# Kernel optimization log

Hardware: AMD Instinct MI355X
Metric: run time of the kernel (lower is better)

## Reference

```python
import jax, jax.numpy as jnp
import numpy as np

N = 8192        # num_drugs
D_EMB = 256     # args.gcn_hidden3 (global encoder input)
D_FEAT = 256    # args.hidden_size (local encoder input)
H1 = H2 = H3 = 256  # args.ff_hidden1/2/3
LOG2 = float(np.log(2.0))
ADJ_DENSITY = 0.01


def _ff(x, w1, b1, w2, b2, w3, b3, ws, bs):
    # FF block: 3-layer ReLU MLP + linear shortcut (FF_local / FF_global)
    h = jax.nn.relu(x @ w1 + b1)
    h = jax.nn.relu(h @ w2 + b2)
    h = jax.nn.relu(h @ w3 + b3)
    return h + x @ ws + bs


def _lin_init(k, fan_in, fan_out):
    s = 1.0 / np.sqrt(fan_in)
    kw, kb = jax.random.split(k)
    w = jax.random.uniform(kw, (fan_in, fan_out), minval=-s, maxval=s, dtype=jnp.float32)
    b = jax.random.uniform(kb, (fan_out,), minval=-s, maxval=s, dtype=jnp.float32)
    return w, b


def setup_inputs() -> dict:
    key = jax.random.key(0)
    ks = jax.random.split(key, 11)
    g_w1, g_b1 = _lin_init(ks[0], D_EMB, H1)
    g_w2, g_b2 = _lin_init(ks[1], H1, H2)
    g_w3, g_b3 = _lin_init(ks[2], H2, H3)
    g_ws, g_bs = _lin_init(ks[3], D_EMB, H3)
    l_w1, l_b1 = _lin_init(ks[4], D_FEAT, H1)
    l_w2, l_b2 = _lin_init(ks[5], H1, H2)
    l_w3, l_b3 = _lin_init(ks[6], H2, H3)
    l_ws, l_bs = _lin_init(ks[7], D_FEAT, H3)
    embeddings = jax.random.normal(ks[8], (N, D_EMB), dtype=jnp.float32)
    features = jax.random.normal(ks[9], (N, D_FEAT), dtype=jnp.float32)
    adj_tensor = (jax.random.uniform(ks[10], (N, N)) < ADJ_DENSITY).astype(jnp.float32)
    return dict(embeddings=embeddings, features=features, adj_tensor=adj_tensor,
                num_drugs=N,
                g_w1=g_w1, g_b1=g_b1, g_w2=g_w2, g_b2=g_b2, g_w3=g_w3, g_b3=g_b3,
                g_ws=g_ws, g_bs=g_bs,
                l_w1=l_w1, l_b1=l_b1, l_w2=l_w2, l_b2=l_b2, l_w3=l_w3, l_b3=l_b3,
                l_ws=l_ws, l_bs=l_bs)


def reference(embeddings, features, adj_tensor,
              g_w1, g_b1, g_w2, g_b2, g_w3, g_b3, g_ws, g_bs,
              l_w1, l_b1, l_w2, l_b2, l_w3, l_b3, l_ws, l_bs,
              num_drugs):
    g_enc = _ff(embeddings, g_w1, g_b1, g_w2, g_b2, g_w3, g_b3, g_ws, g_bs)  # [N, H3]
    l_enc = _ff(features,   l_w1, l_b1, l_w2, l_b2, l_w3, l_b3, l_ws, l_bs)  # [N, H3]
    res = l_enc @ g_enc.T                      # [N, N] pairwise local-global scores
    pos_mask = adj_tensor
    neg_mask = 1.0 - adj_tensor
    # JSD estimator (as in InfoGraph/MIRACLE: mask applied BEFORE the expectation)
    p = res * pos_mask
    E_pos = jnp.sum(LOG2 - jax.nn.softplus(-p)) / num_drugs
    q = res * neg_mask
    E_neg = jnp.sum(jax.nn.softplus(-q) + q - LOG2) / (num_drugs * (num_drugs - 1))
    return E_neg - E_pos  # prior=False -> PRIOR term is 0
```

## Files before the change

kernel.cpp:

```cpp
#include <hip/hip_runtime.h>
#include <hip/hip_bf16.h>
#include <stdint.h>

typedef __bf16 bf16;
typedef __bf16 bf16x8 __attribute__((ext_vector_type(8)));
typedef float f32x4 __attribute__((ext_vector_type(4)));

#define N_DRUGS 8192
#define DIM 256
#define LOG2_C 0.6931471805599453f
#define W_POS (1.0f / 8192.0f)
#define W_NEG (1.0f / (8192.0f * 8191.0f))

__device__ inline void gload_lds16(const void* g, void* l) {
  __builtin_amdgcn_global_load_lds(
      (const __attribute__((address_space(1))) void*)g,
      (__attribute__((address_space(3))) void*)l, 16, 0, 0);
}

__device__ inline int swz(int row, int c) {
  return (c & ~7) | ((c ^ row) & 7);
}

__device__ inline float load_as_f32(const void* p, size_t idx, int dt_bf16) {
  return dt_bf16 ? (float)((const bf16*)p)[idx] : ((const float*)p)[idx];
}

__global__ void detect_dtype(const unsigned short* emb, int* flag) {
  int l = threadIdx.x & 63;
  unsigned short u = emb[2 * l];
  int e = (u >> 7) & 0xFF;
  int plausible = (e >= 96 && e <= 140) || (u == 0);
  unsigned long long m = __ballot(plausible);
  if (l == 0) *flag = (__popcll(m) >= 32) ? 1 : 0;
}

struct P8 { const void* p[8]; };

__global__ __launch_bounds__(256) void transpose_w(P8 srcs, bf16* wt,
                                                   const int* flag) {
  __shared__ bf16 t[32][33];
  const int dt = *flag;
  int m = blockIdx.z;
  const void* src = srcs.p[m];
  bf16* dst = wt + m * 65536;
  int bx = blockIdx.x * 32;
  int by = blockIdx.y * 32;
  int tx = threadIdx.x, ty = threadIdx.y;
#pragma unroll
  for (int i = 0; i < 32; i += 8)
    t[ty + i][tx] = (bf16)load_as_f32(src, (size_t)(by + ty + i) * DIM + bx + tx, dt);
  __syncthreads();
#pragma unroll
  for (int i = 0; i < 32; i += 8)
    dst[(bx + ty + i) * DIM + by + tx] = t[tx][ty + i];
}

struct FFArgs {
  const void *x, *b1, *b2, *b3, *bs;
  const bf16 *wt1, *wt2, *wt3, *wts;
  bf16* out;
};
struct FFBoth { FFArgs a[2]; };

__global__ __launch_bounds__(512) void ff_kernel(FFBoth both, const int* flag) {
  __shared__ __align__(16) bf16 xin[64 * 256];
  __shared__ __align__(16) bf16 cur[64 * 256];
  const FFArgs A = (blockIdx.y == 0) ? both.a[0] : both.a[1];
  const int dt = *flag;

  const int t = threadIdx.x;
  const int w = t >> 6, l = t & 63;
  const int lm = l & 15, lq = l >> 4;
  const int n0 = w * 32;
  const int r0 = blockIdx.x * 64;

  if (dt) {
#pragma unroll
    for (int it = 0; it < 4; ++it) {
      int ci = it * 512 + t, row = ci >> 5, c = ci & 31;
      *(bf16x8*)&xin[row * 256 + swz(row, c) * 8] =
          *(const bf16x8*)&((const bf16*)A.x)[(size_t)(r0 + row) * DIM + c * 8];
    }
  } else {
#pragma unroll
    for (int it = 0; it < 4; ++it) {
      int ci = it * 512 + t, row = ci >> 5, c = ci & 31;
      const float* src = &((const float*)A.x)[(size_t)(r0 + row) * DIM + c * 8];
      bf16x8 v;
#pragma unroll
      for (int e = 0; e < 8; ++e) v[e] = (bf16)src[e];
      *(bf16x8*)&xin[row * 256 + swz(row, c) * 8] = v;
    }
  }
  __syncthreads();

  f32x4 acc[4][2];
  const f32x4 fz = {0.f, 0.f, 0.f, 0.f};

  auto compute = [&](const bf16* src, const bf16* wt) {
#pragma unroll
    for (int i = 0; i < 4; ++i)
#pragma unroll
      for (int j = 0; j < 2; ++j) acc[i][j] = fz;
#pragma unroll
    for (int ks = 0; ks < 256; ks += 32) {
      bf16x8 af[4], bfr[2];
#pragma unroll
      for (int i = 0; i < 4; ++i) {
        int row = i * 16 + lm;
        af[i] = *(const bf16x8*)&src[row * 256 + swz(row, (ks >> 3) + lq) * 8];
      }
#pragma unroll
      for (int j = 0; j < 2; ++j) {
        int n = n0 + j * 16 + lm;
        bfr[j] = *(const bf16x8*)&wt[n * DIM + ks + lq * 8];
      }
#pragma unroll
      for (int i = 0; i < 4; ++i)
#pragma unroll
        for (int j = 0; j < 2; ++j)
          acc[i][j] = __builtin_amdgcn_mfma_f32_16x16x32_bf16(af[i], bfr[j],
                                                              acc[i][j], 0, 0, 0);
    }
  };

  auto store_relu = [&](const void* bias) {
    __syncthreads();
#pragma unroll
    for (int j = 0; j < 2; ++j) {
      int col = n0 + j * 16 + lm;
      float bj = load_as_f32(bias, col, dt);
      int cc = col >> 3, cw = col & 7;
#pragma unroll
      for (int i = 0; i < 4; ++i)
#pragma unroll
        for (int r = 0; r < 4; ++r) {
          int row = i * 16 + lq * 4 + r;
          float v = fmaxf(acc[i][j][r] + bj, 0.f);
          cur[row * 256 + swz(row, cc) * 8 + cw] = (bf16)v;
        }
    }
    __syncthreads();
  };

  compute(xin, A.wt1); store_relu(A.b1);
  compute(cur, A.wt2); store_relu(A.b2);
  compute(cur, A.wt3); store_relu(A.b3);
  compute(xin, A.wts);

#pragma unroll
  for (int j = 0; j < 2; ++j) {
    int col = n0 + j * 16 + lm;
    float bj = load_as_f32(A.bs, col, dt);
    int cc = col >> 3, cw = col & 7;
#pragma unroll
    for (int i = 0; i < 4; ++i)
#pragma unroll
      for (int r = 0; r < 4; ++r) {
        int row = i * 16 + lq * 4 + r;
        float h3 = (float)cur[row * 256 + swz(row, cc) * 8 + cw];
        float v = acc[i][j][r] + bj + h3;
        A.out[(size_t)(r0 + row) * DIM + col] = (bf16)v;
      }
  }
}

__global__ __launch_bounds__(256) void gemm_reduce(const bf16* __restrict__ Lenc,
                                                   const bf16* __restrict__ Genc,
                                                   const void* __restrict__ adj,
                                                   float* accum, const int* flag) {
  __shared__ __align__(16) bf16 smem[2 * 128 * 64];
  __shared__ float red[8];
  bf16* At = smem;
  bf16* Bt = smem + 128 * 64;

  const int dt = *flag;
  const int t = threadIdx.x;
  const int w = t >> 6, l = t & 63;
  const int wr = w >> 1, wc = w & 1;
  const int lm = l & 15, lq = l >> 4;
  const int row0 = blockIdx.y * 128;
  const int col0 = blockIdx.x * 128;

  f32x4 acc[4][4];
  const f32x4 fz = {0.f, 0.f, 0.f, 0.f};
#pragma unroll
  for (int i = 0; i < 4; ++i)
#pragma unroll
    for (int j = 0; j < 4; ++j) acc[i][j] = fz;

  for (int kk = 0; kk < 256; kk += 64) {
    __syncthreads();
#pragma unroll
    for (int it = 0; it < 4; ++it) {
      int ci = it * 256 + t;
      int row = ci >> 3, cs = ci & 7;
      int cg = swz(row, cs);
      bf16* lbase = &At[(it * 256 + w * 64) * 8];
      gload_lds16(&Lenc[(size_t)(row0 + row) * DIM + kk + cg * 8], lbase);
      bf16* lbase2 = &Bt[(it * 256 + w * 64) * 8];
      gload_lds16(&Genc[(size_t)(col0 + row) * DIM + kk + cg * 8], lbase2);
    }
    __syncthreads();
#pragma unroll
    for (int ks = 0; ks < 64; ks += 32) {
      bf16x8 af[4], bfr[4];
#pragma unroll
      for (int i = 0; i < 4; ++i) {
        int row = wr * 64 + i * 16 + lm;
        af[i] = *(const bf16x8*)&At[row * 64 + swz(row, (ks >> 3) + lq) * 8];
      }
#pragma unroll
      for (int j = 0; j < 4; ++j) {
        int row = wc * 64 + j * 16 + lm;
        bfr[j] = *(const bf16x8*)&Bt[row * 64 + swz(row, (ks >> 3) + lq) * 8];
      }
#pragma unroll
      for (int i = 0; i < 4; ++i)
#pragma unroll
        for (int j = 0; j < 4; ++j)
          acc[i][j] = __builtin_amdgcn_mfma_f32_16x16x32_bf16(af[i], bfr[j],
                                                              acc[i][j], 0, 0, 0);
    }
  }

  float lsum = 0.f;
  __syncthreads();

  auto jsd = [&](float res, float a) {
    float s = fmaxf(res, 0.f) + __logf(1.f + __expf(-fabsf(res)));
    float vneg = (s - LOG2_C) * W_NEG;
    float vpos = (s - res - LOG2_C) * W_POS;
    return (a > 0.5f) ? vpos : vneg;
  };

  if (dt) {
    const bf16* adjB = (const bf16*)adj;
#pragma unroll
    for (int it = 0; it < 8; ++it) {
      int ci = it * 256 + t;
      int row = ci >> 4, c = ci & 15;
      int cg = c ^ (row & 15);
      bf16* lbase = &smem[(it * 256 + w * 64) * 8];
      gload_lds16(&adjB[(size_t)(row0 + row) * N_DRUGS + col0 + cg * 8], lbase);
    }
    __syncthreads();
#pragma unroll
    for (int i = 0; i < 4; ++i)
#pragma unroll
      for (int r = 0; r < 4; ++r) {
        int row = wr * 64 + i * 16 + lq * 4 + r;
#pragma unroll
        for (int j = 0; j < 4; ++j) {
          int col = wc * 64 + j * 16 + lm;
          int slot = (col >> 3) ^ (row & 15);
          float a = (float)smem[(row * 16 + slot) * 8 + (col & 7)];
          lsum += jsd(acc[i][j][r], a);
        }
      }
  } else {
    const float* adjF = (const float*)adj;
    float* AdjL = (float*)smem;
    for (int h = 0; h < 2; ++h) {
      if (h) __syncthreads();
#pragma unroll
      for (int it = 0; it < 8; ++it) {
        int ci = it * 256 + t;
        int r4 = ci >> 5, c = ci & 31;
        int pr = (r4 >> 5) * 64 + h * 32 + (r4 & 31);
        int cg = (c & 16) | ((c ^ (r4 & 15)) & 15);
        float* lbase = &AdjL[(it * 256 + w * 64) * 4];
        gload_lds16(&adjF[(size_t)(row0 + pr) * N_DRUGS + col0 + cg * 4], lbase);
      }
      __syncthreads();
#pragma unroll
      for (int ii = 0; ii < 2; ++ii) {
        int i = 2 * h + ii;
#pragma unroll
        for (int r = 0; r < 4; ++r) {
          int r4 = wr * 32 + ii * 16 + lq * 4 + r;
#pragma unroll
          for (int j = 0; j < 4; ++j) {
            int col = wc * 64 + j * 16 + lm;
            int cread = col >> 2;
            int slot = (cread & 16) | ((cread ^ (r4 & 15)) & 15);
            float a = AdjL[(r4 * 32 + slot) * 4 + (col & 3)];
            lsum += jsd(acc[i][j][r], a);
          }
        }
      }
      if (h == 0) __syncthreads();
    }
  }

#pragma unroll
  for (int off = 32; off > 0; off >>= 1) lsum += __shfl_down(lsum, off, 64);
  if (l == 0) red[w] = lsum;
  __syncthreads();
  if (t == 0) atomicAdd(accum, red[0] + red[1] + red[2] + red[3]);
}

__global__ void finalize_k(const float* accum, unsigned int* out) {
  if (threadIdx.x == 0 && blockIdx.x == 0) {
    float v = *accum;
    union { bf16 h; unsigned short u; } cv;
    cv.h = (bf16)v;
    out[0] = ((unsigned int)cv.u << 16) | cv.u;
  }
}

extern "C" void kernel_launch(void* const* d_in, const int* in_sizes, int n_in,
                              void* d_out, int out_size, void* d_ws, size_t ws_size,
                              hipStream_t stream) {
  const void* embeddings = d_in[0];
  const void* features   = d_in[1];
  const void* adj        = d_in[2];

  char* ws = (char*)d_ws;
  float* accum = (float*)ws;
  int* flag = (int*)(ws + 64);
  bf16* wt   = (bf16*)(ws + 1024);
  bf16* genc = (bf16*)(ws + 1024 + 8 * 65536 * 2);
  bf16* lenc = (bf16*)(ws + 1024 + 8 * 65536 * 2 + (size_t)N_DRUGS * DIM * 2);

  hipMemsetAsync(accum, 0, sizeof(float), stream);

  detect_dtype<<<1, 64, 0, stream>>>((const unsigned short*)embeddings, flag);

  P8 srcs;
  srcs.p[0] = d_in[4];  srcs.p[1] = d_in[6];  srcs.p[2] = d_in[8];  srcs.p[3] = d_in[10];
  srcs.p[4] = d_in[12]; srcs.p[5] = d_in[14]; srcs.p[6] = d_in[16]; srcs.p[7] = d_in[18];
  transpose_w<<<dim3(8, 8, 8), dim3(32, 8), 0, stream>>>(srcs, wt, flag);

  FFBoth fb;
  fb.a[0] = FFArgs{embeddings, d_in[5], d_in[7], d_in[9], d_in[11],
                   wt + 0 * 65536, wt + 1 * 65536, wt + 2 * 65536, wt + 3 * 65536,
                   genc};
  fb.a[1] = FFArgs{features, d_in[13], d_in[15], d_in[17], d_in[19],
                   wt + 4 * 65536, wt + 5 * 65536, wt + 6 * 65536, wt + 7 * 65536,
                   lenc};
  ff_kernel<<<dim3(128, 2), 512, 0, stream>>>(fb, flag);

  gemm_reduce<<<dim3(64, 64), 256, 0, stream>>>(lenc, genc, adj, accum, flag);

  finalize_k<<<1, 64, 0, stream>>>(accum, (unsigned int*)d_out);
}
```

Baseline: 455.2 us.

## Inline dtype sniffing, fuse finalize, swizzle tile order, stream adjacency loads

Removes the separate dtype-detection and finalize kernels: each kernel now sniffs the input dtype itself, and the last GEMM block, found through an atomic counter, writes the output. Block indices are remapped into 8x8 chunks so neighbouring blocks reuse the L2-resident Lenc/Genc tiles. Adjacency loads get a cache-policy aux bit (2), meant to act as a non-temporal/streaming hint, and the mask test becomes an integer compare. The cost is extra per-block sniffing loads and an atomic/threadfence tail in every block.

```diff
diff --git a/kernel.cpp b/kernel.cpp
--- a/kernel.cpp
+++ b/kernel.cpp
@@ -12,10 +12,11 @@
 #define W_POS (1.0f / 8192.0f)
 #define W_NEG (1.0f / (8192.0f * 8191.0f))
 
+template <int AUX = 0>
 __device__ inline void gload_lds16(const void* g, void* l) {
   __builtin_amdgcn_global_load_lds(
       (const __attribute__((address_space(1))) void*)g,
-      (__attribute__((address_space(3))) void*)l, 16, 0, 0);
+      (__attribute__((address_space(3))) void*)l, 16, 0, AUX);
 }
 
 __device__ inline int swz(int row, int c) {
@@ -26,21 +27,22 @@
   return dt_bf16 ? (float)((const bf16*)p)[idx] : ((const float*)p)[idx];
 }
 
-__global__ void detect_dtype(const unsigned short* emb, int* flag) {
+__device__ inline int sniff_dt(const void* x) {
+  const unsigned short* u16p = (const unsigned short*)x;
   int l = threadIdx.x & 63;
-  unsigned short u = emb[2 * l];
+  unsigned short u = u16p[2 * l];
   int e = (u >> 7) & 0xFF;
   int plausible = (e >= 96 && e <= 140) || (u == 0);
   unsigned long long m = __ballot(plausible);
-  if (l == 0) *flag = (__popcll(m) >= 32) ? 1 : 0;
+  return (__popcll(m) >= 32) ? 1 : 0;
 }
 
 struct P8 { const void* p[8]; };
 
 __global__ __launch_bounds__(256) void transpose_w(P8 srcs, bf16* wt,
-                                                   const int* flag) {
+                                                   const void* emb) {
   __shared__ bf16 t[32][33];
-  const int dt = *flag;
+  const int dt = sniff_dt(emb);
   int m = blockIdx.z;
   const void* src = srcs.p[m];
   bf16* dst = wt + m * 65536;
@@ -63,11 +65,11 @@
 };
 struct FFBoth { FFArgs a[2]; };
 
-__global__ __launch_bounds__(512) void ff_kernel(FFBoth both, const int* flag) {
+__global__ __launch_bounds__(512) void ff_kernel(FFBoth both) {
   __shared__ __align__(16) bf16 xin[64 * 256];
   __shared__ __align__(16) bf16 cur[64 * 256];
   const FFArgs A = (blockIdx.y == 0) ? both.a[0] : both.a[1];
-  const int dt = *flag;
+  const int dt = sniff_dt(A.x);
 
   const int t = threadIdx.x;
   const int w = t >> 6, l = t & 63;
@@ -166,22 +168,27 @@
   }
 }
 
-__global__ __launch_bounds__(256) void gemm_reduce(const bf16* __restrict__ Lenc,
-                                                   const bf16* __restrict__ Genc,
-                                                   const void* __restrict__ adj,
-                                                   float* accum, const int* flag) {
+__global__ __launch_bounds__(256) void gemm_reduce(
+    const bf16* __restrict__ Lenc, const bf16* __restrict__ Genc,
+    const void* __restrict__ adj, const void* __restrict__ emb,
+    float* accum, unsigned* counter, unsigned* out) {
   __shared__ __align__(16) bf16 smem[2 * 128 * 64];
-  __shared__ float red[8];
+  __shared__ float red[4];
   bf16* At = smem;
   bf16* Bt = smem + 128 * 64;
 
-  const int dt = *flag;
+  const int dt = sniff_dt(emb);
   const int t = threadIdx.x;
   const int w = t >> 6, l = t & 63;
   const int wr = w >> 1, wc = w & 1;
   const int lm = l & 15, lq = l >> 4;
-  const int row0 = blockIdx.y * 128;
-  const int col0 = blockIdx.x * 128;
+
+  int sid = blockIdx.x + 64 * blockIdx.y;
+  int chunk = sid >> 6, l6 = sid & 63;
+  int bx = (chunk & 7) * 8 + (l6 & 7);
+  int by = (chunk >> 3) * 8 + (l6 >> 3);
+  const int row0 = by * 128;
+  const int col0 = bx * 128;
 
   f32x4 acc[4][4];
   const f32x4 fz = {0.f, 0.f, 0.f, 0.f};
@@ -198,9 +205,9 @@
       int row = ci >> 3, cs = ci & 7;
       int cg = swz(row, cs);
       bf16* lbase = &At[(it * 256 + w * 64) * 8];
-      gload_lds16(&Lenc[(size_t)(row0 + row) * DIM + kk + cg * 8], lbase);
+      gload_lds16<0>(&Lenc[(size_t)(row0 + row) * DIM + kk + cg * 8], lbase);
       bf16* lbase2 = &Bt[(it * 256 + w * 64) * 8];
-      gload_lds16(&Genc[(size_t)(col0 + row) * DIM + kk + cg * 8], lbase2);
+      gload_lds16<0>(&Genc[(size_t)(col0 + row) * DIM + kk + cg * 8], lbase2);
     }
     __syncthreads();
 #pragma unroll
@@ -228,11 +235,11 @@
   float lsum = 0.f;
   __syncthreads();
 
-  auto jsd = [&](float res, float a) {
+  auto jsd = [&](float res, int pos) {
     float s = fmaxf(res, 0.f) + __logf(1.f + __expf(-fabsf(res)));
     float vneg = (s - LOG2_C) * W_NEG;
     float vpos = (s - res - LOG2_C) * W_POS;
-    return (a > 0.5f) ? vpos : vneg;
+    return pos ? vpos : vneg;
   };
 
   if (dt) {
@@ -243,9 +250,10 @@
       int row = ci >> 4, c = ci & 15;
       int cg = c ^ (row & 15);
       bf16* lbase = &smem[(it * 256 + w * 64) * 8];
-      gload_lds16(&adjB[(size_t)(row0 + row) * N_DRUGS + col0 + cg * 8], lbase);
-    }
-    __syncthreads();
+      gload_lds16<2>(&adjB[(size_t)(row0 + row) * N_DRUGS + col0 + cg * 8], lbase);
+    }
+    __syncthreads();
+    const unsigned short* sm16 = (const unsigned short*)smem;
 #pragma unroll
     for (int i = 0; i < 4; ++i)
 #pragma unroll
@@ -255,8 +263,8 @@
         for (int j = 0; j < 4; ++j) {
           int col = wc * 64 + j * 16 + lm;
           int slot = (col >> 3) ^ (row & 15);
-          float a = (float)smem[(row * 16 + slot) * 8 + (col & 7)];
-          lsum += jsd(acc[i][j][r], a);
+          int pos = sm16[(row * 16 + slot) * 8 + (col & 7)] != 0;
+          lsum += jsd(acc[i][j][r], pos);
         }
       }
   } else {
@@ -271,7 +279,7 @@
         int pr = (r4 >> 5) * 64 + h * 32 + (r4 & 31);
         int cg = (c & 16) | ((c ^ (r4 & 15)) & 15);
         float* lbase = &AdjL[(it * 256 + w * 64) * 4];
-        gload_lds16(&adjF[(size_t)(row0 + pr) * N_DRUGS + col0 + cg * 4], lbase);
+        gload_lds16<2>(&adjF[(size_t)(row0 + pr) * N_DRUGS + col0 + cg * 4], lbase);
       }
       __syncthreads();
 #pragma unroll
@@ -285,8 +293,8 @@
             int col = wc * 64 + j * 16 + lm;
             int cread = col >> 2;
             int slot = (cread & 16) | ((cread ^ (r4 & 15)) & 15);
-            float a = AdjL[(r4 * 32 + slot) * 4 + (col & 3)];
-            lsum += jsd(acc[i][j][r], a);
+            int pos = AdjL[(r4 * 32 + slot) * 4 + (col & 3)] != 0.f;
+            lsum += jsd(acc[i][j][r], pos);
           }
         }
       }
@@ -298,15 +306,17 @@
   for (int off = 32; off > 0; off >>= 1) lsum += __shfl_down(lsum, off, 64);
   if (l == 0) red[w] = lsum;
   __syncthreads();
-  if (t == 0) atomicAdd(accum, red[0] + red[1] + red[2] + red[3]);
-}
-
-__global__ void finalize_k(const float* accum, unsigned int* out) {
-  if (threadIdx.x == 0 && blockIdx.x == 0) {
-    float v = *accum;
-    union { bf16 h; unsigned short u; } cv;
-    cv.h = (bf16)v;
-    out[0] = ((unsigned int)cv.u << 16) | cv.u;
+  if (t == 0) {
+    atomicAdd(accum, red[0] + red[1] + red[2] + red[3]);
+    __threadfence();
+    unsigned old = atomicAdd(counter, 1u);
+    if (old == 64 * 64 - 1) {
+      __threadfence();
+      float v = atomicAdd(accum, 0.0f);
+      union { bf16 h; unsigned short u; } cv;
+      cv.h = (bf16)v;
+      out[0] = ((unsigned)cv.u << 16) | cv.u;
+    }
   }
 }
 
@@ -319,19 +329,17 @@
 
   char* ws = (char*)d_ws;
   float* accum = (float*)ws;
-  int* flag = (int*)(ws + 64);
+  unsigned* counter = (unsigned*)(ws + 4);
   bf16* wt   = (bf16*)(ws + 1024);
   bf16* genc = (bf16*)(ws + 1024 + 8 * 65536 * 2);
   bf16* lenc = (bf16*)(ws + 1024 + 8 * 65536 * 2 + (size_t)N_DRUGS * DIM * 2);
 
-  hipMemsetAsync(accum, 0, sizeof(float), stream);
-
-  detect_dtype<<<1, 64, 0, stream>>>((const unsigned short*)embeddings, flag);
+  hipMemsetAsync(ws, 0, 8, stream);
 
   P8 srcs;
   srcs.p[0] = d_in[4];  srcs.p[1] = d_in[6];  srcs.p[2] = d_in[8];  srcs.p[3] = d_in[10];
   srcs.p[4] = d_in[12]; srcs.p[5] = d_in[14]; srcs.p[6] = d_in[16]; srcs.p[7] = d_in[18];
-  transpose_w<<<dim3(8, 8, 8), dim3(32, 8), 0, stream>>>(srcs, wt, flag);
+  transpose_w<<<dim3(8, 8, 8), dim3(32, 8), 0, stream>>>(srcs, wt, embeddings);
 
   FFBoth fb;
   fb.a[0] = FFArgs{embeddings, d_in[5], d_in[7], d_in[9], d_in[11],
@@ -340,9 +348,8 @@
   fb.a[1] = FFArgs{features, d_in[13], d_in[15], d_in[17], d_in[19],
                    wt + 4 * 65536, wt + 5 * 65536, wt + 6 * 65536, wt + 7 * 65536,
                    lenc};
-  ff_kernel<<<dim3(128, 2), 512, 0, stream>>>(fb, flag);
-
-  gemm_reduce<<<dim3(64, 64), 256, 0, stream>>>(lenc, genc, adj, accum, flag);
-
-  finalize_k<<<1, 64, 0, stream>>>(accum, (unsigned int*)d_out);
-}
+  ff_kernel<<<dim3(128, 2), 512, 0, stream>>>(fb);
+
+  gemm_reduce<<<dim3(64, 64), 256, 0, stream>>>(lenc, genc, adj, embeddings,
+                                                accum, counter, (unsigned*)d_out);
+}
```

Measured after the change: 569.9 us. 1.25x slower.
